# Performance work log

Hardware: AMD Instinct MI355X
Metric: run time of the kernel (lower is better)

Reference implementation:

```python
import jax, jax.numpy as jnp
import numpy as np

EMBED_DIM = 1024
N_HEADS = 16
HEAD_DIM = EMBED_DIM // N_HEADS
EPS = 1e-6


def setup_inputs() -> dict:
    key = jax.random.key(0)
    k_x, k_wqkv, k_bqkv, k_wo, k_bo = jax.random.split(key, 5)
    B, T, C = 2, 2048, EMBED_DIM
    s = 1.0 / np.sqrt(C)
    return {
        "x": jax.random.normal(k_x, (B, T, C), dtype=jnp.float32),
        "w_qkv": jax.random.normal(k_wqkv, (C, 3 * C), dtype=jnp.float32) * s,
        "b_qkv": jax.random.normal(k_bqkv, (3 * C,), dtype=jnp.float32) * s,
        "w_out": jax.random.normal(k_wo, (C, C), dtype=jnp.float32) * s,
        "b_out": jax.random.normal(k_bo, (C,), dtype=jnp.float32) * s,
    }


def reference(x, w_qkv, b_qkv, w_out, b_out):
    B, T, C = x.shape
    H, D = N_HEADS, HEAD_DIM
    qkv = x @ w_qkv + b_qkv                       # [B,T,3C]
    q, k, v = jnp.split(qkv, 3, axis=-1)
    # [B,H,T,D]
    q = q.reshape(B, T, H, D).transpose(0, 2, 1, 3)
    k = k.reshape(B, T, H, D).transpose(0, 2, 1, 3)
    v = v.reshape(B, T, H, D).transpose(0, 2, 1, 3)
    dot = jnp.einsum("bhqd,bhkd->bhqk", q, k)     # [B,H,T,T]
    q_sq = jnp.sum(q * q, axis=-1)[..., :, None]  # [B,H,T,1]
    k_sq = jnp.sum(k * k, axis=-1)[..., None, :]  # [B,H,1,T]
    scores = (dot * dot) / (q_sq + k_sq - 2.0 * dot + EPS)
    causal = jnp.tril(jnp.ones((T, T), dtype=bool))
    scores = jnp.where(causal, scores, -jnp.inf)
    attn = jax.nn.softmax(scores, axis=-1)
    out = jnp.einsum("bhqk,bhkd->bhqd", attn, v)  # [B,H,T,D]
    out = out.transpose(0, 2, 1, 3).reshape(B, T, C)
    return out @ w_out + b_out
```

## Files before the change

### kernel.cpp

```cpp
#include <hip/hip_runtime.h>
#include <stdint.h>


#define TSEQ 2048
#define BATCH 2

typedef _Float16 f16x8 __attribute__((ext_vector_type(8)));
typedef float f32x4 __attribute__((ext_vector_type(4)));

#define MFMA16(a, b, c) __builtin_amdgcn_mfma_f32_16x16x32_f16(a, b, c, 0, 0, 0)

__device__ __forceinline__ unsigned short f2h(float f) {
  union { _Float16 h; unsigned short u; } v;
  v.h = (_Float16)f;
  return v.u;
}
__device__ __forceinline__ float h2f(unsigned short u) {
  union { unsigned short u; _Float16 h; } v;
  v.u = u;
  return (float)v.h;
}
__device__ __forceinline__ unsigned int pack2h(float lo, float hi) {
  return (unsigned int)f2h(lo) | ((unsigned int)f2h(hi) << 16);
}
__device__ __forceinline__ float sumsq_u32(unsigned int u) {
  float lo = h2f(u & 0xffffu);
  float hi = h2f(u >> 16);
  return lo * lo + hi * hi;
}
__device__ __forceinline__ void async_ld16(const void* g, const void* l) {
  __builtin_amdgcn_global_load_lds((const __attribute__((address_space(1))) void*)g,
                                   (__attribute__((address_space(3))) void*)l,
                                   16, 0, 0);
}

__global__ __launch_bounds__(256) void cvt_x(const float* __restrict__ src,
                                             unsigned short* __restrict__ dst) {
  const int i = (blockIdx.x * 256 + threadIdx.x) * 8;
  const float4 a = *(const float4*)(src + i);
  const float4 b = *(const float4*)(src + i + 4);
  uint4 o;
  o.x = pack2h(a.x, a.y); o.y = pack2h(a.z, a.w);
  o.z = pack2h(b.x, b.y); o.w = pack2h(b.z, b.w);
  *(uint4*)(dst + i) = o;
}

__global__ __launch_bounds__(256) void transpose_w(const float* __restrict__ src,
                                                   unsigned short* __restrict__ dst,
                                                   int K, int N) {
  __shared__ unsigned short tile[32][33];
  const int tx = threadIdx.x, ty = threadIdx.y;
  const int nb = blockIdx.x * 32, kb = blockIdx.y * 32;
#pragma unroll
  for (int i = 0; i < 4; i++)
    tile[ty + 8 * i][tx] = f2h(src[(size_t)(kb + ty + 8 * i) * N + nb + tx]);
  __syncthreads();
#pragma unroll
  for (int i = 0; i < 4; i++)
    dst[(size_t)(nb + ty + 8 * i) * K + kb + tx] = tile[tx][ty + 8 * i];
}

template <bool OUT_F32>
__global__ __launch_bounds__(256) void gemm_bt(const unsigned short* __restrict__ A,
                                               const unsigned short* __restrict__ Bt,
                                               const float* __restrict__ bias,
                                               void* __restrict__ Cp,
                                               int N, int K) {
  __shared__ __attribute__((aligned(16))) unsigned short Atile[128 * 32];
  __shared__ __attribute__((aligned(16))) unsigned short Btile[128 * 32];
  const int tid = threadIdx.x;
  const int w = tid >> 6, lane = tid & 63;
  const int quad = lane >> 4, l15 = lane & 15;
  const int m0 = blockIdx.y * 128, n0 = blockIdx.x * 128;
  const int wr = w >> 1, wc = w & 1;
  f32x4 acc[4][4] = {};
  for (int kt = 0; kt < K; kt += 32) {
    __syncthreads();
#pragma unroll
    for (int it = 0; it < 2; it++) {
      const int c = it * 256 + tid;
      const int row = c >> 2, kc = c & 3;
      async_ld16(A + (size_t)(m0 + row) * K + kt + kc * 8,
                 &Atile[(size_t)(it * 256 + w * 64) * 8]);
      async_ld16(Bt + (size_t)(n0 + row) * K + kt + kc * 8,
                 &Btile[(size_t)(it * 256 + w * 64) * 8]);
    }
    __syncthreads();
    f16x8 af[4], bfr[4];
#pragma unroll
    for (int i = 0; i < 4; i++)
      af[i] = *(const f16x8*)&Atile[(wr * 64 + i * 16 + l15) * 32 + quad * 8];
#pragma unroll
    for (int j = 0; j < 4; j++)
      bfr[j] = *(const f16x8*)&Btile[(wc * 64 + j * 16 + l15) * 32 + quad * 8];
#pragma unroll
    for (int i = 0; i < 4; i++)
#pragma unroll
      for (int j = 0; j < 4; j++)
        acc[i][j] = MFMA16(af[i], bfr[j], acc[i][j]);
  }
#pragma unroll
  for (int j = 0; j < 4; j++) {
    const int n = n0 + wc * 64 + j * 16 + l15;
    const float bv = bias[n];
#pragma unroll
    for (int i = 0; i < 4; i++) {
      const int mb = m0 + wr * 64 + i * 16 + quad * 4;
#pragma unroll
      for (int r = 0; r < 4; r++) {
        if constexpr (OUT_F32)
          ((float*)Cp)[(size_t)(mb + r) * N + n] = acc[i][j][r] + bv;
        else
          ((unsigned short*)Cp)[(size_t)(mb + r) * N + n] = f2h(acc[i][j][r] + bv);
      }
    }
  }
}

__global__ __launch_bounds__(256, 4) void yat_attn(const unsigned short* __restrict__ qkv,
                                                   unsigned short* __restrict__ outp) {
  __shared__ __attribute__((aligned(16))) unsigned short Qp[64 * 72];
  __shared__ __attribute__((aligned(16))) unsigned short Kp[64 * 72];
  __shared__ __attribute__((aligned(16))) unsigned short Vt[64 * 72];
  __shared__ __attribute__((aligned(16))) unsigned short Pl[64 * 72];
  __shared__ float qsq[64], ksq[64], bcast[64];
  const int tid = threadIdx.x;
  const int w = tid >> 6, lane = tid & 63;
  const int quad = lane >> 4, l15 = lane & 15;
  const int bh = blockIdx.x, b = bh >> 4, h = bh & 15;
  const int y = blockIdx.y;
  const int qt = (y < 8) ? 31 - y : (y < 16) ? y - 8 : (y < 24) ? 39 - y : y - 16;
  const unsigned short* base = qkv + (size_t)b * TSEQ * 3072 + h * 64;
  const int t = tid >> 2, dc = (tid & 3) * 16;
  const int d0 = tid & 31, tg8 = tid >> 5;

  {
    const unsigned short* g = base + (size_t)(qt * 64 + t) * 3072 + dc;
    uint4 v0 = *(const uint4*)g;
    uint4 v1 = *(const uint4*)(g + 8);
    *(uint4*)&Qp[t * 72 + dc] = v0;
    *(uint4*)&Qp[t * 72 + dc + 8] = v1;
    float s = sumsq_u32(v0.x) + sumsq_u32(v0.y) + sumsq_u32(v0.z) + sumsq_u32(v0.w) +
              sumsq_u32(v1.x) + sumsq_u32(v1.y) + sumsq_u32(v1.z) + sumsq_u32(v1.w);
    s += __shfl_xor(s, 1);
    s += __shfl_xor(s, 2);
    if ((tid & 3) == 0) qsq[t] = s;
  }

  f32x4 accO[4] = {};
  float m_r[4] = {0.f, 0.f, 0.f, 0.f};
  float l_r[4] = {0.f, 0.f, 0.f, 0.f};

  uint4 kreg0, kreg1;
  unsigned int vreg[8];
  {
    const unsigned short* gk = base + 1024 + (size_t)t * 3072 + dc;
    kreg0 = *(const uint4*)gk;
    kreg1 = *(const uint4*)(gk + 8);
    const unsigned short* gv = base + 2048 + (size_t)(tg8 * 8) * 3072 + 2 * d0;
#pragma unroll
    for (int s = 0; s < 8; s++)
      vreg[s] = *(const unsigned int*)(gv + (size_t)s * 3072);
  }

  for (int kt = 0; kt <= qt; kt++) {
    __syncthreads();
    {
      *(uint4*)&Kp[t * 72 + dc] = kreg0;
      *(uint4*)&Kp[t * 72 + dc + 8] = kreg1;
      float s = sumsq_u32(kreg0.x) + sumsq_u32(kreg0.y) + sumsq_u32(kreg0.z) +
                sumsq_u32(kreg0.w) + sumsq_u32(kreg1.x) + sumsq_u32(kreg1.y) +
                sumsq_u32(kreg1.z) + sumsq_u32(kreg1.w);
      s += __shfl_xor(s, 1);
      s += __shfl_xor(s, 2);
      if ((tid & 3) == 0) ksq[t] = s;
      uint4 LO, HI;
      LO.x = (vreg[0] & 0xffffu) | (vreg[1] << 16);
      LO.y = (vreg[2] & 0xffffu) | (vreg[3] << 16);
      LO.z = (vreg[4] & 0xffffu) | (vreg[5] << 16);
      LO.w = (vreg[6] & 0xffffu) | (vreg[7] << 16);
      HI.x = (vreg[0] >> 16) | (vreg[1] & 0xffff0000u);
      HI.y = (vreg[2] >> 16) | (vreg[3] & 0xffff0000u);
      HI.z = (vreg[4] >> 16) | (vreg[5] & 0xffff0000u);
      HI.w = (vreg[6] >> 16) | (vreg[7] & 0xffff0000u);
      *(uint4*)&Vt[(2 * d0) * 72 + tg8 * 8] = LO;
      *(uint4*)&Vt[(2 * d0 + 1) * 72 + tg8 * 8] = HI;
    }
    if (kt < qt) {
      const unsigned short* gk = base + 1024 + (size_t)((kt + 1) * 64 + t) * 3072 + dc;
      kreg0 = *(const uint4*)gk;
      kreg1 = *(const uint4*)(gk + 8);
      const unsigned short* gv =
          base + 2048 + (size_t)((kt + 1) * 64 + tg8 * 8) * 3072 + 2 * d0;
#pragma unroll
      for (int s = 0; s < 8; s++)
        vreg[s] = *(const unsigned int*)(gv + (size_t)s * 3072);
    }
    __syncthreads();

    f32x4 accS[4] = {};
    const f16x8 aq0 = *(const f16x8*)&Qp[(w * 16 + l15) * 72 + quad * 8];
    const f16x8 aq1 = *(const f16x8*)&Qp[(w * 16 + l15) * 72 + 32 + quad * 8];
#pragma unroll
    for (int nt = 0; nt < 4; nt++) {
      const f16x8 bk0 = *(const f16x8*)&Kp[(nt * 16 + l15) * 72 + quad * 8];
      const f16x8 bk1 = *(const f16x8*)&Kp[(nt * 16 + l15) * 72 + 32 + quad * 8];
      accS[nt] = MFMA16(aq0, bk0, accS[nt]);
      accS[nt] = MFMA16(aq1, bk1, accS[nt]);
    }
    const bool diag = (kt == qt);
    float pval[4][4];
    float tmax[4] = {0.f, 0.f, 0.f, 0.f};
#pragma unroll
    for (int nt = 0; nt < 4; nt++) {
#pragma unroll
      for (int r = 0; r < 4; r++) {
        const int ql = w * 16 + quad * 4 + r;
        const int tl = nt * 16 + l15;
        const float d = accS[nt][r];
        const float den = qsq[ql] + ksq[tl] - 2.f * d + 1e-6f;
        float s = d * d * __builtin_amdgcn_rcpf(den);
        if (diag && tl > ql) s = -1e30f;
        pval[nt][r] = s;
        tmax[r] = fmaxf(tmax[r], s);
      }
    }
#pragma unroll
    for (int r = 0; r < 4; r++) {
      tmax[r] = fmaxf(tmax[r], __shfl_xor(tmax[r], 1));
      tmax[r] = fmaxf(tmax[r], __shfl_xor(tmax[r], 2));
      tmax[r] = fmaxf(tmax[r], __shfl_xor(tmax[r], 4));
      tmax[r] = fmaxf(tmax[r], __shfl_xor(tmax[r], 8));
    }
    float alpha[4];
#pragma unroll
    for (int r = 0; r < 4; r++) {
      const float mn = fmaxf(m_r[r], tmax[r]);
      alpha[r] = __expf(m_r[r] - mn);
      m_r[r] = mn;
    }
#pragma unroll
    for (int nt = 0; nt < 4; nt++)
#pragma unroll
      for (int r = 0; r < 4; r++)
        pval[nt][r] = __expf(pval[nt][r] - m_r[r]);
#pragma unroll
    for (int r = 0; r < 4; r++) {
      float su = pval[0][r] + pval[1][r] + pval[2][r] + pval[3][r];
      su += __shfl_xor(su, 1);
      su += __shfl_xor(su, 2);
      su += __shfl_xor(su, 4);
      su += __shfl_xor(su, 8);
      l_r[r] = l_r[r] * alpha[r] + su;
    }
#pragma unroll
    for (int nt = 0; nt < 4; nt++)
#pragma unroll
      for (int r = 0; r < 4; r++)
        Pl[(w * 16 + quad * 4 + r) * 72 + nt * 16 + l15] = f2h(pval[nt][r]);
    if (l15 == 0) {
#pragma unroll
      for (int r = 0; r < 4; r++) bcast[w * 16 + quad * 4 + r] = alpha[r];
    }
    __syncthreads();

    const float am = bcast[w * 16 + l15];
#pragma unroll
    for (int i = 0; i < 4; i++) {
      accO[i][0] *= am; accO[i][1] *= am; accO[i][2] *= am; accO[i][3] *= am;
    }
    const f16x8 bp0 = *(const f16x8*)&Pl[(w * 16 + l15) * 72 + quad * 8];
    const f16x8 bp1 = *(const f16x8*)&Pl[(w * 16 + l15) * 72 + 32 + quad * 8];
#pragma unroll
    for (int i = 0; i < 4; i++) {
      const f16x8 av0 = *(const f16x8*)&Vt[(i * 16 + l15) * 72 + quad * 8];
      const f16x8 av1 = *(const f16x8*)&Vt[(i * 16 + l15) * 72 + 32 + quad * 8];
      accO[i] = MFMA16(av0, bp0, accO[i]);
      accO[i] = MFMA16(av1, bp1, accO[i]);
    }
  }

  __syncthreads();
  if (l15 == 0) {
#pragma unroll
    for (int r = 0; r < 4; r++) bcast[w * 16 + quad * 4 + r] = l_r[r];
  }
  __syncthreads();
  const float linv = 1.0f / bcast[w * 16 + l15];
#pragma unroll
  for (int i = 0; i < 4; i++)
#pragma unroll
    for (int r = 0; r < 4; r++)
      Qp[(w * 16 + l15) * 72 + i * 16 + quad * 4 + r] = f2h(accO[i][r] * linv);
  __syncthreads();
  {
    uint4 o0 = *(const uint4*)&Qp[t * 72 + dc];
    uint4 o1 = *(const uint4*)&Qp[t * 72 + dc + 8];
    unsigned short* g = outp + (size_t)(b * TSEQ + qt * 64 + t) * 1024 + h * 64 + dc;
    *(uint4*)g = o0;
    *(uint4*)(g + 8) = o1;
  }
}

extern "C" void kernel_launch(void* const* d_in, const int* in_sizes, int n_in,
                              void* d_out, int out_size, void* d_ws, size_t ws_size,
                              hipStream_t stream) {
  (void)in_sizes; (void)n_in; (void)out_size; (void)ws_size;
  const float* x     = (const float*)d_in[0];
  const float* w_qkv = (const float*)d_in[1];
  const float* b_qkv = (const float*)d_in[2];
  const float* w_out = (const float*)d_in[3];
  const float* b_out = (const float*)d_in[4];
  float* out = (float*)d_out;

  unsigned short* wqkvT  = (unsigned short*)d_ws;
  unsigned short* woT    = wqkvT + (size_t)3072 * 1024;
  unsigned short* qkvws  = woT + (size_t)1024 * 1024;
  unsigned short* xh     = qkvws + (size_t)4096 * 3072;
  unsigned short* attnws = xh;

  cvt_x<<<dim3(4096 * 1024 / (256 * 8)), 256, 0, stream>>>(x, xh);
  transpose_w<<<dim3(3072 / 32, 1024 / 32), dim3(32, 8), 0, stream>>>(w_qkv, wqkvT, 1024, 3072);
  transpose_w<<<dim3(1024 / 32, 1024 / 32), dim3(32, 8), 0, stream>>>(w_out, woT, 1024, 1024);
  gemm_bt<false><<<dim3(3072 / 128, 4096 / 128), 256, 0, stream>>>(xh, wqkvT, b_qkv, qkvws, 3072, 1024);
  yat_attn<<<dim3(BATCH * 16, 32), 256, 0, stream>>>(qkvws, attnws);
  gemm_bt<true><<<dim3(1024 / 128, 4096 / 128), 256, 0, stream>>>(attnws, woT, b_out, out, 1024, 1024);
}
```

Baseline: 226.3 us.

## Use DPP row max, MFMA row sums, hoisted Q fragments, narrower out-proj tiles

The attention kernel replaces shuffle-based row-max reductions with DPP row_shr steps and computes softmax row sums with an MFMA against a ones vector instead of shuffle reductions. Q fragments are loaded once before the key loop rather than every iteration, and the final bcast round-trip for l is dropped. The output projection GEMM is templated on N tile width and launched with 64-wide tiles, doubling the block count for the small N=1024 GEMM to fill more CUs. This trades a few extra MFMAs for fewer cross-lane shuffles. It relies on the DPP row_shr max producing the full row max in the lane that needs it.

```diff
diff --git a/kernel.cpp b/kernel.cpp
--- a/kernel.cpp
+++ b/kernel.cpp
@@ -32,6 +32,19 @@
   __builtin_amdgcn_global_load_lds((const __attribute__((address_space(1))) void*)g,
                                    (__attribute__((address_space(3))) void*)l,
                                    16, 0, 0);
+}
+template <int CTRL>
+__device__ __forceinline__ float dpp_max_step(float x) {
+  float y = __uint_as_float((unsigned)__builtin_amdgcn_update_dpp(
+      0, (int)__float_as_uint(x), CTRL, 0xf, 0xf, true));
+  return fmaxf(x, y);
+}
+__device__ __forceinline__ float dpp_row_max(float x) {
+  x = dpp_max_step<0x121>(x);
+  x = dpp_max_step<0x122>(x);
+  x = dpp_max_step<0x124>(x);
+  x = dpp_max_step<0x128>(x);
+  return x;
 }
 
 __global__ __launch_bounds__(256) void cvt_x(const float* __restrict__ src,
@@ -60,48 +73,53 @@
     dst[(size_t)(nb + ty + 8 * i) * K + kb + tx] = tile[tx][ty + 8 * i];
 }
 
-template <bool OUT_F32>
+template <int TN, bool OUT_F32>
 __global__ __launch_bounds__(256) void gemm_bt(const unsigned short* __restrict__ A,
                                                const unsigned short* __restrict__ Bt,
                                                const float* __restrict__ bias,
                                                void* __restrict__ Cp,
                                                int N, int K) {
   __shared__ __attribute__((aligned(16))) unsigned short Atile[128 * 32];
-  __shared__ __attribute__((aligned(16))) unsigned short Btile[128 * 32];
+  __shared__ __attribute__((aligned(16))) unsigned short Btile[TN * 32];
+  constexpr int NJ = TN / 32;
   const int tid = threadIdx.x;
   const int w = tid >> 6, lane = tid & 63;
   const int quad = lane >> 4, l15 = lane & 15;
-  const int m0 = blockIdx.y * 128, n0 = blockIdx.x * 128;
+  const int m0 = blockIdx.y * 128, n0 = blockIdx.x * TN;
   const int wr = w >> 1, wc = w & 1;
-  f32x4 acc[4][4] = {};
+  const int nwc = wc * (TN / 2);
+  f32x4 acc[4][NJ] = {};
   for (int kt = 0; kt < K; kt += 32) {
     __syncthreads();
 #pragma unroll
     for (int it = 0; it < 2; it++) {
       const int c = it * 256 + tid;
-      const int row = c >> 2, kc = c & 3;
-      async_ld16(A + (size_t)(m0 + row) * K + kt + kc * 8,
+      async_ld16(A + (size_t)(m0 + (c >> 2)) * K + kt + (c & 3) * 8,
                  &Atile[(size_t)(it * 256 + w * 64) * 8]);
-      async_ld16(Bt + (size_t)(n0 + row) * K + kt + kc * 8,
+    }
+#pragma unroll
+    for (int it = 0; it < TN / 64; it++) {
+      const int c = it * 256 + tid;
+      async_ld16(Bt + (size_t)(n0 + (c >> 2)) * K + kt + (c & 3) * 8,
                  &Btile[(size_t)(it * 256 + w * 64) * 8]);
     }
     __syncthreads();
-    f16x8 af[4], bfr[4];
+    f16x8 af[4], bfr[NJ];
 #pragma unroll
     for (int i = 0; i < 4; i++)
       af[i] = *(const f16x8*)&Atile[(wr * 64 + i * 16 + l15) * 32 + quad * 8];
 #pragma unroll
-    for (int j = 0; j < 4; j++)
-      bfr[j] = *(const f16x8*)&Btile[(wc * 64 + j * 16 + l15) * 32 + quad * 8];
+    for (int j = 0; j < NJ; j++)
+      bfr[j] = *(const f16x8*)&Btile[(nwc + j * 16 + l15) * 32 + quad * 8];
 #pragma unroll
     for (int i = 0; i < 4; i++)
 #pragma unroll
-      for (int j = 0; j < 4; j++)
+      for (int j = 0; j < NJ; j++)
         acc[i][j] = MFMA16(af[i], bfr[j], acc[i][j]);
   }
 #pragma unroll
-  for (int j = 0; j < 4; j++) {
-    const int n = n0 + wc * 64 + j * 16 + l15;
+  for (int j = 0; j < NJ; j++) {
+    const int n = n0 + nwc + j * 16 + l15;
     const float bv = bias[n];
 #pragma unroll
     for (int i = 0; i < 4; i++) {
@@ -146,10 +164,15 @@
     s += __shfl_xor(s, 2);
     if ((tid & 3) == 0) qsq[t] = s;
   }
+  __syncthreads();
+  const f16x8 aq0 = *(const f16x8*)&Qp[(w * 16 + l15) * 72 + quad * 8];
+  const f16x8 aq1 = *(const f16x8*)&Qp[(w * 16 + l15) * 72 + 32 + quad * 8];
+  const f16x8 onesf = {(_Float16)1.f, (_Float16)1.f, (_Float16)1.f, (_Float16)1.f,
+                       (_Float16)1.f, (_Float16)1.f, (_Float16)1.f, (_Float16)1.f};
 
   f32x4 accO[4] = {};
   float m_r[4] = {0.f, 0.f, 0.f, 0.f};
-  float l_r[4] = {0.f, 0.f, 0.f, 0.f};
+  float l_acc = 0.f;
 
   uint4 kreg0, kreg1;
   unsigned int vreg[8];
@@ -199,8 +222,6 @@
     __syncthreads();
 
     f32x4 accS[4] = {};
-    const f16x8 aq0 = *(const f16x8*)&Qp[(w * 16 + l15) * 72 + quad * 8];
-    const f16x8 aq1 = *(const f16x8*)&Qp[(w * 16 + l15) * 72 + 32 + quad * 8];
 #pragma unroll
     for (int nt = 0; nt < 4; nt++) {
       const f16x8 bk0 = *(const f16x8*)&Kp[(nt * 16 + l15) * 72 + quad * 8];
@@ -225,17 +246,10 @@
         tmax[r] = fmaxf(tmax[r], s);
       }
     }
+    float alpha[4];
 #pragma unroll
     for (int r = 0; r < 4; r++) {
-      tmax[r] = fmaxf(tmax[r], __shfl_xor(tmax[r], 1));
-      tmax[r] = fmaxf(tmax[r], __shfl_xor(tmax[r], 2));
-      tmax[r] = fmaxf(tmax[r], __shfl_xor(tmax[r], 4));
-      tmax[r] = fmaxf(tmax[r], __shfl_xor(tmax[r], 8));
-    }
-    float alpha[4];
-#pragma unroll
-    for (int r = 0; r < 4; r++) {
-      const float mn = fmaxf(m_r[r], tmax[r]);
+      const float mn = fmaxf(m_r[r], dpp_row_max(tmax[r]));
       alpha[r] = __expf(m_r[r] - mn);
       m_r[r] = mn;
     }
@@ -243,21 +257,8 @@
     for (int nt = 0; nt < 4; nt++)
 #pragma unroll
       for (int r = 0; r < 4; r++)
-        pval[nt][r] = __expf(pval[nt][r] - m_r[r]);
-#pragma unroll
-    for (int r = 0; r < 4; r++) {
-      float su = pval[0][r] + pval[1][r] + pval[2][r] + pval[3][r];
-      su += __shfl_xor(su, 1);
-      su += __shfl_xor(su, 2);
-      su += __shfl_xor(su, 4);
-      su += __shfl_xor(su, 8);
-      l_r[r] = l_r[r] * alpha[r] + su;
-    }
-#pragma unroll
-    for (int nt = 0; nt < 4; nt++)
-#pragma unroll
-      for (int r = 0; r < 4; r++)
-        Pl[(w * 16 + quad * 4 + r) * 72 + nt * 16 + l15] = f2h(pval[nt][r]);
+        Pl[(w * 16 + quad * 4 + r) * 72 + nt * 16 + l15] =
+            f2h(__expf(pval[nt][r] - m_r[r]));
     if (l15 == 0) {
 #pragma unroll
       for (int r = 0; r < 4; r++) bcast[w * 16 + quad * 4 + r] = alpha[r];
@@ -271,6 +272,9 @@
     }
     const f16x8 bp0 = *(const f16x8*)&Pl[(w * 16 + l15) * 72 + quad * 8];
     const f16x8 bp1 = *(const f16x8*)&Pl[(w * 16 + l15) * 72 + 32 + quad * 8];
+    f32x4 accL = {};
+    accL = MFMA16(onesf, bp0, accL);
+    accL = MFMA16(onesf, bp1, accL);
 #pragma unroll
     for (int i = 0; i < 4; i++) {
       const f16x8 av0 = *(const f16x8*)&Vt[(i * 16 + l15) * 72 + quad * 8];
@@ -278,15 +282,11 @@
       accO[i] = MFMA16(av0, bp0, accO[i]);
       accO[i] = MFMA16(av1, bp1, accO[i]);
     }
+    l_acc = l_acc * am + accL[0];
   }
 
   __syncthreads();
-  if (l15 == 0) {
-#pragma unroll
-    for (int r = 0; r < 4; r++) bcast[w * 16 + quad * 4 + r] = l_r[r];
-  }
-  __syncthreads();
-  const float linv = 1.0f / bcast[w * 16 + l15];
+  const float linv = 1.0f / l_acc;
 #pragma unroll
   for (int i = 0; i < 4; i++)
 #pragma unroll
@@ -322,7 +322,7 @@
   cvt_x<<<dim3(4096 * 1024 / (256 * 8)), 256, 0, stream>>>(x, xh);
   transpose_w<<<dim3(3072 / 32, 1024 / 32), dim3(32, 8), 0, stream>>>(w_qkv, wqkvT, 1024, 3072);
   transpose_w<<<dim3(1024 / 32, 1024 / 32), dim3(32, 8), 0, stream>>>(w_out, woT, 1024, 1024);
-  gemm_bt<false><<<dim3(3072 / 128, 4096 / 128), 256, 0, stream>>>(xh, wqkvT, b_qkv, qkvws, 3072, 1024);
+  gemm_bt<128, false><<<dim3(3072 / 128, 4096 / 128), 256, 0, stream>>>(xh, wqkvT, b_qkv, qkvws, 3072, 1024);
   yat_attn<<<dim3(BATCH * 16, 32), 256, 0, stream>>>(qkvws, attnws);
-  gemm_bt<true><<<dim3(1024 / 128, 4096 / 128), 256, 0, stream>>>(attnws, woT, b_out, out, 1024, 1024);
-}
+  gemm_bt<64, true><<<dim3(1024 / 64, 4096 / 128), 256, 0, stream>>>(attnws, woT, b_out, out, 1024, 1024);
+}
```

Result: faster. 205.5 us (-9.2%).
